# Performance work log

Hardware: AMD Instinct MI355X
Metric: run time of the kernel (lower is better)

The kernel has to match this reference:

```python
import jax, jax.numpy as jnp
import numpy as np

D_MODEL = 1024
N_HEADS = 1  # original code's final .view only works for n_heads == 1 (unprojected V has dim d_model per head)
HEAD_DIM = D_MODEL // N_HEADS
N, LEN_Q, LEN_IN = 8, 1024, 4096


def setup_inputs() -> dict:
    key = jax.random.key(0)
    ks = jax.random.split(key, 7)
    s = 1.0 / np.sqrt(D_MODEL)  # linear-layer style init scale
    return {
        "query": jax.random.normal(ks[0], (N, LEN_Q, D_MODEL), dtype=jnp.float32),
        "input_flatten": jax.random.normal(ks[1], (N, LEN_IN, D_MODEL), dtype=jnp.float32),
        "input_padding_mask": jax.random.randint(ks[2], (N, LEN_IN), 0, 2).astype(bool),
        "Wq": jax.random.normal(ks[3], (D_MODEL, D_MODEL), dtype=jnp.float32) * s,
        "bq": jnp.zeros((D_MODEL,), dtype=jnp.float32),
        "Wk": jax.random.normal(ks[4], (D_MODEL, D_MODEL), dtype=jnp.float32) * s,
        "bk": jnp.zeros((D_MODEL,), dtype=jnp.float32),
        "Wo": jax.random.normal(ks[5], (D_MODEL, D_MODEL), dtype=jnp.float32) * s,
        "bo": jnp.zeros((D_MODEL,), dtype=jnp.float32),
    }


def reference(query, input_flatten, input_padding_mask, Wq, bq, Wk, bk, Wo, bo):
    n, len_q, _ = query.shape
    len_in = input_flatten.shape[1]
    # projections (torch Linear: x @ W^T + b)
    Q = (query @ Wq.T + bq).reshape(n, len_q, N_HEADS, HEAD_DIM).transpose(0, 2, 1, 3)
    K = (input_flatten @ Wk.T + bk).reshape(n, len_in, N_HEADS, HEAD_DIM).transpose(0, 2, 1, 3)
    # unscaled attention scores (original applies no 1/sqrt(d))
    scores = jnp.einsum("nhqd,nhkd->nhqk", Q, K)  # (N, H, Lq, Lk)
    scores = jnp.where(input_padding_mask[:, None, None, :], -jnp.inf, scores)
    attn = jax.nn.softmax(scores, axis=-1)
    # V is the UNPROJECTED input, replicated per head (dim = d_model)
    V = jnp.broadcast_to(input_flatten[:, None], (n, N_HEADS, len_in, D_MODEL))
    out = jnp.einsum("nhql,nhld->nhqd", attn, V)  # (N, H, Lq, d_model)
    out = out.transpose(0, 2, 1, 3).reshape(n, len_q, D_MODEL)  # valid since N_HEADS == 1
    return out @ Wo.T + bo
```

## Files before the change

### kernel.cpp

```cpp
#include <hip/hip_runtime.h>
#include <math.h>


using short8 = __attribute__((ext_vector_type(8))) short;
using f32x4  = __attribute__((ext_vector_type(4))) float;

__device__ inline ushort f2h_u(float f) {
    _Float16 h = (_Float16)f;
    return __builtin_bit_cast(ushort, h);
}
__device__ inline float h2f(ushort u) {
    return (float)__builtin_bit_cast(_Float16, u);
}
__device__ inline void split2h(float x, ushort& h, ushort& l) {
    const ushort hu = f2h_u(x);
    h = hu;
    l = f2h_u(x - h2f(hu));
}

__global__ __launch_bounds__(256)
void bias_proj_k(const float* __restrict__ bq, const float* __restrict__ Wk,
                 float* __restrict__ bp)
{
    const int j = blockIdx.x * 256 + threadIdx.x;
    float s = 0.f;
    for (int d = 0; d < 1024; ++d) s = fmaf(bq[d], Wk[d * 1024 + j], s);
    bp[j] = s;
}

__global__ __launch_bounds__(256)
void split_k(const float* __restrict__ x, ushort* __restrict__ hi,
             ushort* __restrict__ lo, int n4)
{
    for (int i = blockIdx.x * 256 + threadIdx.x; i < n4; i += gridDim.x * 256) {
        const float4 v = reinterpret_cast<const float4*>(x)[i];
        ushort4 h, l;
        split2h(v.x, h.x, l.x); split2h(v.y, h.y, l.y);
        split2h(v.z, h.z, l.z); split2h(v.w, h.w, l.w);
        reinterpret_cast<ushort4*>(hi)[i] = h;
        if (lo) reinterpret_cast<ushort4*>(lo)[i] = l;
    }
}

__global__ __launch_bounds__(256)
void trans_split_k(const float* __restrict__ in, ushort* __restrict__ oh,
                   ushort* __restrict__ ol, int R, int C)
{
    __shared__ float ts[32][33];
    const int t = threadIdx.x, tx = t & 31, tg = t >> 5;
    const int r0 = blockIdx.y * 32, c0 = blockIdx.x * 32;
    #pragma unroll
    for (int i = 0; i < 4; ++i) {
        const int r = tg * 4 + i;
        ts[r][tx] = in[(size_t)(r0 + r) * C + c0 + tx];
    }
    __syncthreads();
    #pragma unroll
    for (int i = 0; i < 4; ++i) {
        const int c = tg * 4 + i;
        ushort h, l; split2h(ts[tx][c], h, l);
        const size_t o = (size_t)(c0 + c) * R + r0 + tx;
        oh[o] = h;
        if (ol) ol[o] = l;
    }
}

__global__ __launch_bounds__(256)
void prep_input_k(const float* __restrict__ in, ushort* __restrict__ i2,
                  ushort* __restrict__ vt, int LI, int D, long long bs)
{
    __shared__ float ts[32][33];
    const int t = threadIdx.x;
    const int tx8 = t & 7, ty = t >> 3;
    const int r0 = blockIdx.y * 32, c0 = blockIdx.x * 32;
    const long long z = blockIdx.z;
    in += z * bs; i2 += z * bs * 2; vt += z * bs;

    const float4 v = *reinterpret_cast<const float4*>(
        &in[(size_t)(r0 + ty) * D + c0 + tx8 * 4]);
    ushort4 h, l;
    split2h(v.x, h.x, l.x); split2h(v.y, h.y, l.y);
    split2h(v.z, h.z, l.z); split2h(v.w, h.w, l.w);
    const size_t rbase = (size_t)(r0 + ty) * 2048 + c0 + tx8 * 4;
    *reinterpret_cast<ushort4*>(&i2[rbase]) = h;
    *reinterpret_cast<ushort4*>(&i2[rbase + 1024]) = l;
    ts[ty][tx8 * 4 + 0] = v.x; ts[ty][tx8 * 4 + 1] = v.y;
    ts[ty][tx8 * 4 + 2] = v.z; ts[ty][tx8 * 4 + 3] = v.w;
    __syncthreads();
    const int tx = t & 31, tg = t >> 5;
    #pragma unroll
    for (int i = 0; i < 4; ++i) {
        const int c = tg * 4 + i;
        vt[(size_t)(c0 + c) * LI + r0 + tx] = f2h_u(ts[tx][c]);
    }
}

__global__ __launch_bounds__(256)
void softmax_f16_k(const float* __restrict__ S, const int* __restrict__ mask,
                   ushort* __restrict__ P)
{
    const int t = threadIdx.x;
    const size_t row = (size_t)blockIdx.y * gridDim.x + blockIdx.x;
    const float* srow = S + row * 4096;
    ushort* prow = P + row * 4096;
    mask += (size_t)blockIdx.y * 4096;
    float4 v[4];
    float lmax = -INFINITY;
    #pragma unroll
    for (int c = 0; c < 4; ++c) {
        const int idx = c * 1024 + t * 4;
        v[c] = *reinterpret_cast<const float4*>(&srow[idx]);
        const int4 m4 = *reinterpret_cast<const int4*>(&mask[idx]);
        if (m4.x) v[c].x = -INFINITY;
        if (m4.y) v[c].y = -INFINITY;
        if (m4.z) v[c].z = -INFINITY;
        if (m4.w) v[c].w = -INFINITY;
        lmax = fmaxf(lmax, fmaxf(fmaxf(v[c].x, v[c].y), fmaxf(v[c].z, v[c].w)));
    }
    #pragma unroll
    for (int off = 32; off > 0; off >>= 1)
        lmax = fmaxf(lmax, __shfl_xor(lmax, off));
    __shared__ float redm[4], reds[4];
    if ((t & 63) == 0) redm[t >> 6] = lmax;
    __syncthreads();
    const float bmax = fmaxf(fmaxf(redm[0], redm[1]), fmaxf(redm[2], redm[3]));
    float lsum = 0.f;
    #pragma unroll
    for (int c = 0; c < 4; ++c) {
        v[c].x = __expf(v[c].x - bmax);
        v[c].y = __expf(v[c].y - bmax);
        v[c].z = __expf(v[c].z - bmax);
        v[c].w = __expf(v[c].w - bmax);
        lsum += (v[c].x + v[c].y) + (v[c].z + v[c].w);
    }
    #pragma unroll
    for (int off = 32; off > 0; off >>= 1)
        lsum += __shfl_xor(lsum, off);
    if ((t & 63) == 0) reds[t >> 6] = lsum;
    __syncthreads();
    const float Z = (reds[0] + reds[1]) + (reds[2] + reds[3]);
    const float inv = 1.0f / Z;
    #pragma unroll
    for (int c = 0; c < 4; ++c) {
        const int idx = c * 1024 + t * 4;
        ushort4 o;
        o.x = f2h_u(v[c].x * inv); o.y = f2h_u(v[c].y * inv);
        o.z = f2h_u(v[c].z * inv); o.w = f2h_u(v[c].w * inv);
        *reinterpret_cast<ushort4*>(&prow[idx]) = o;
    }
}

template<int TR>
__device__ inline void stage_one(const ushort* __restrict__ g, int ld, int r0,
                                 int k0, ushort* ldsbase, int w, int l)
{
    constexpr int ISS = TR / 64;
    #pragma unroll
    for (int q = 0; q < ISS; ++q) {
        const int idx = (w * ISS + q) * 64 + l;
        const int row = idx >> 2;
        const int gslot = (idx & 3) ^ ((idx >> 3) & 3);
        const ushort* src = g + (size_t)(r0 + row) * ld + k0 + gslot * 8;
        ushort* dst = ldsbase + (size_t)(w * ISS + q) * 512;
        __builtin_amdgcn_global_load_lds(
            (const __attribute__((address_space(1))) void*)src,
            (__attribute__((address_space(3))) void*)dst, 16, 0, 0);
    }
}

template<int BM, int BN, int AS, int BS, int OUTMODE>
__global__ __launch_bounds__(256, 2)
void mfma_gemm_k(const ushort* __restrict__ Ah, const ushort* __restrict__ Al,
                 const ushort* __restrict__ Bh, const ushort* __restrict__ Bl,
                 const float* __restrict__ bias,
                 float* __restrict__ Cf, ushort* __restrict__ Ch,
                 ushort* __restrict__ Cl,
                 int K, int lda, int ldb, int ldc,
                 long long bsA, long long bsB, long long bsC)
{
    constexpr int FM = BM / 32, FN = BN / 32;
    constexpr int AU = AS * BM * 32;
    constexpr int TILE_U = AU + BS * BN * 32;
    __shared__ __align__(16) ushort lds[2][TILE_U];

    const long long zb = blockIdx.z;
    Ah += zb * bsA; Bh += zb * bsB;
    if constexpr (AS == 2) Al += zb * bsA;
    if constexpr (BS == 2) Bl += zb * bsB;

    const int t = threadIdx.x;
    const int l = t & 63, w = t >> 6;
    const int lr = l & 15, ls = l >> 4;
    const int i0 = blockIdx.y * BM, j0 = blockIdx.x * BN;
    const int wr = (w >> 1) * (BM / 2), wc = (w & 1) * (BN / 2);
    const int swu = (ls ^ ((lr >> 1) & 3)) * 8;

    f32x4 acc[FM][FN] = {};
    const int nk = K >> 5;

    auto stage = [&](int buf, int kt) {
        const int k0 = kt << 5;
        ushort* base = &lds[buf][0];
        stage_one<BM>(Ah, lda, i0, k0, base, w, l);
        if constexpr (AS == 2) stage_one<BM>(Al, lda, i0, k0, base + BM * 32, w, l);
        stage_one<BN>(Bh, ldb, j0, k0, base + AU, w, l);
        if constexpr (BS == 2) stage_one<BN>(Bl, ldb, j0, k0, base + AU + BN * 32, w, l);
    };

    stage(0, 0);
    for (int kt = 0; kt < nk; ++kt) {
        __syncthreads();
        const int buf = kt & 1;
        if (kt + 1 < nk) stage(buf ^ 1, kt + 1);
        const ushort* base = &lds[buf][0];

        short8 ah[FM], bh[FN];
        #pragma unroll
        for (int fi = 0; fi < FM; ++fi)
            ah[fi] = *reinterpret_cast<const short8*>(
                base + (wr + fi * 16 + lr) * 32 + swu);
        #pragma unroll
        for (int fj = 0; fj < FN; ++fj)
            bh[fj] = *reinterpret_cast<const short8*>(
                base + AU + (wc + fj * 16 + lr) * 32 + swu);

        #pragma unroll
        for (int fi = 0; fi < FM; ++fi)
            #pragma unroll
            for (int fj = 0; fj < FN; ++fj)
                acc[fi][fj] = __builtin_amdgcn_mfma_f32_16x16x32_f16(
                    ah[fi], bh[fj], acc[fi][fj], 0, 0, 0);

        if constexpr (BS == 2) {
            short8 bl[FN];
            #pragma unroll
            for (int fj = 0; fj < FN; ++fj)
                bl[fj] = *reinterpret_cast<const short8*>(
                    base + AU + BN * 32 + (wc + fj * 16 + lr) * 32 + swu);
            #pragma unroll
            for (int fi = 0; fi < FM; ++fi)
                #pragma unroll
                for (int fj = 0; fj < FN; ++fj)
                    acc[fi][fj] = __builtin_amdgcn_mfma_f32_16x16x32_f16(
                        ah[fi], bl[fj], acc[fi][fj], 0, 0, 0);
        }
        if constexpr (AS == 2) {
            short8 al[FM];
            #pragma unroll
            for (int fi = 0; fi < FM; ++fi)
                al[fi] = *reinterpret_cast<const short8*>(
                    base + BM * 32 + (wr + fi * 16 + lr) * 32 + swu);
            #pragma unroll
            for (int fi = 0; fi < FM; ++fi)
                #pragma unroll
                for (int fj = 0; fj < FN; ++fj)
                    acc[fi][fj] = __builtin_amdgcn_mfma_f32_16x16x32_f16(
                        al[fi], bh[fj], acc[fi][fj], 0, 0, 0);
        }
    }

    #pragma unroll
    for (int fj = 0; fj < FN; ++fj) {
        const int gc = j0 + wc + fj * 16 + lr;
        const float bv = bias ? bias[gc] : 0.0f;
        #pragma unroll
        for (int fi = 0; fi < FM; ++fi) {
            const int gr = i0 + wr + fi * 16 + ls * 4;
            #pragma unroll
            for (int r = 0; r < 4; ++r) {
                const float v = acc[fi][fj][r] + bv;
                const size_t o = zb * bsC + (size_t)(gr + r) * ldc + gc;
                if constexpr (OUTMODE == 0) {
                    Cf[o] = v;
                } else if constexpr (OUTMODE == 1) {
                    Ch[o] = f2h_u(v);
                } else {
                    ushort h, lo2; split2h(v, h, lo2);
                    Ch[o] = h;
                    Cl[o] = lo2;
                }
            }
        }
    }
}

__global__ __launch_bounds__(512, 2)
void gemm256_k(const ushort* __restrict__ A, const ushort* __restrict__ B,
               float* __restrict__ Cf,
               int K, int lda, int ldb, int ldc, int kmaskA,
               long long bsA, long long bsB, long long bsC,
               int gx, int gy)
{
    extern __shared__ ushort lds[];
    const int tid = threadIdx.x;
    const int w = tid >> 6, l = tid & 63;
    const int lr = l & 15, ls = l >> 4;
    const int wr = (w >> 2) * 128, wc = (w & 3) * 64;

    const int nwg = gridDim.x;
    const int q8 = nwg >> 3;
    const int swz = (blockIdx.x & 7) * q8 + (blockIdx.x >> 3);
    const int pt = gx * gy;
    const int z = swz / pt;
    const int r2 = swz - z * pt;
    const int by = r2 / gx, bx = r2 - by * gx;
    const int i0 = by * 256, j0 = bx * 256;

    A += (long long)z * bsA;
    B += (long long)z * bsB;

    const int swu = (ls ^ ((lr >> 1) & 3)) * 8;
    const int kmaskB = K - 1;

    f32x4 acc[8][4] = {};
    const int nk = K >> 6;

    auto stage = [&](const ushort* g, int ld, int row0, int kbase, int kmask, int reg) {
        ushort* base = lds + reg * 8192;
        #pragma unroll
        for (int q2 = 0; q2 < 2; ++q2) {
            const int s = (w * 2 + q2) * 64 + l;
            const int row = s >> 2;
            const int gslot = (s & 3) ^ ((row >> 1) & 3);
            const ushort* src = g + (size_t)(row0 + row) * ld + ((kbase + gslot * 8) & kmask);
            __builtin_amdgcn_global_load_lds(
                (const __attribute__((address_space(1))) void*)src,
                (__attribute__((address_space(3))) void*)(base + s * 8), 16, 0, 0);
        }
    };

    stage(A, lda, i0, 0,  kmaskA, 0);
    stage(B, ldb, j0, 0,  kmaskB, 1);
    stage(A, lda, i0, 32, kmaskA, 2);
    stage(B, ldb, j0, 32, kmaskB, 3);
    stage(A, lda, i0, 64, kmaskA, 4);
    stage(B, ldb, j0, 64, kmaskB, 5);
    asm volatile("s_waitcnt vmcnt(8)" ::: "memory");
    __builtin_amdgcn_s_barrier();

#define MFMA16(MH)                                                          \
    __builtin_amdgcn_s_setprio(1);                                          \
    _Pragma("unroll")                                                       \
    for (int i = 0; i < 4; ++i)                                             \
        _Pragma("unroll")                                                   \
        for (int j = 0; j < 4; ++j)                                         \
            acc[(MH)*4 + i][j] = __builtin_amdgcn_mfma_f32_16x16x32_f16(    \
                af[i], bf[j], acc[(MH)*4 + i][j], 0, 0, 0);                 \
    __builtin_amdgcn_s_setprio(0);

    for (int t = 0; t < nk; ++t) {
        const int b = t & 1;
        const int t1 = (t + 1 < nk) ? t + 1 : 0;
        const int t2 = (t + 2 < nk) ? t + 2 : t + 2 - nk;
        const int cb = b * 4, rb = (b ^ 1) * 4;
        const ushort* RA0 = lds + (cb + 0) * 8192;
        const ushort* RB0 = lds + (cb + 1) * 8192;
        const ushort* RA1 = lds + (cb + 2) * 8192;
        const ushort* RB1 = lds + (cb + 3) * 8192;

        short8 af[4], bf[4];

        #pragma unroll
        for (int i = 0; i < 4; ++i)
            af[i] = *reinterpret_cast<const short8*>(RA0 + (wr + i * 16 + lr) * 32 + swu);
        #pragma unroll
        for (int j = 0; j < 4; ++j)
            bf[j] = *reinterpret_cast<const short8*>(RB0 + (wc + j * 16 + lr) * 32 + swu);
        stage(A, lda, i0, t1 * 64 + 32, kmaskA, rb + 2);
        __builtin_amdgcn_s_barrier();
        asm volatile("s_waitcnt lgkmcnt(0)" ::: "memory");
        __builtin_amdgcn_sched_barrier(0);
        MFMA16(0)
        __builtin_amdgcn_s_barrier();

        #pragma unroll
        for (int i = 0; i < 4; ++i)
            af[i] = *reinterpret_cast<const short8*>(RA0 + (wr + 64 + i * 16 + lr) * 32 + swu);
        stage(B, ldb, j0, t1 * 64 + 32, kmaskB, rb + 3);
        asm volatile("s_waitcnt vmcnt(8)" ::: "memory");
        __builtin_amdgcn_s_barrier();
        asm volatile("s_waitcnt lgkmcnt(0)" ::: "memory");
        __builtin_amdgcn_sched_barrier(0);
        MFMA16(1)
        __builtin_amdgcn_s_barrier();

        #pragma unroll
        for (int i = 0; i < 4; ++i)
            af[i] = *reinterpret_cast<const short8*>(RA1 + (wr + i * 16 + lr) * 32 + swu);
        #pragma unroll
        for (int j = 0; j < 4; ++j)
            bf[j] = *reinterpret_cast<const short8*>(RB1 + (wc + j * 16 + lr) * 32 + swu);
        stage(A, lda, i0, t2 * 64, kmaskA, cb + 0);
        __builtin_amdgcn_s_barrier();
        asm volatile("s_waitcnt lgkmcnt(0)" ::: "memory");
        __builtin_amdgcn_sched_barrier(0);
        MFMA16(0)
        __builtin_amdgcn_s_barrier();

        #pragma unroll
        for (int i = 0; i < 4; ++i)
            af[i] = *reinterpret_cast<const short8*>(RA1 + (wr + 64 + i * 16 + lr) * 32 + swu);
        stage(B, ldb, j0, t2 * 64, kmaskB, cb + 1);
        asm volatile("s_waitcnt vmcnt(8)" ::: "memory");
        __builtin_amdgcn_s_barrier();
        asm volatile("s_waitcnt lgkmcnt(0)" ::: "memory");
        __builtin_amdgcn_sched_barrier(0);
        MFMA16(1)
        __builtin_amdgcn_s_barrier();
    }
#undef MFMA16

    asm volatile("s_waitcnt vmcnt(0)" ::: "memory");

    #pragma unroll
    for (int a = 0; a < 8; ++a) {
        const int gr0 = i0 + wr + (a >> 2) * 64 + (a & 3) * 16 + ls * 4;
        #pragma unroll
        for (int j = 0; j < 4; ++j) {
            const int gc = j0 + wc + j * 16 + lr;
            #pragma unroll
            for (int r = 0; r < 4; ++r)
                Cf[(long long)z * bsC + (size_t)(gr0 + r) * ldc + gc] = acc[a][j][r];
        }
    }
}

extern "C" void kernel_launch(void* const* d_in, const int* in_sizes, int n_in,
                              void* d_out, int out_size, void* d_ws, size_t ws_size,
                              hipStream_t stream)
{
    (void)in_sizes; (void)n_in; (void)out_size;
    const int NB = 8, LQ = 1024, LI = 4096, D = 1024;
    const long long sQD = (long long)LQ * D;
    const long long sID = (long long)LI * D;
    const long long sQI = (long long)LQ * LI;

    const float* query = (const float*)d_in[0];
    const float* input = (const float*)d_in[1];
    const int* mask = (const int*)d_in[2];
    const float* Wq = (const float*)d_in[3];
    const float* bq = (const float*)d_in[4];
    const float* Wk = (const float*)d_in[5];
    const float* Wo = (const float*)d_in[7];
    const float* bo = (const float*)d_in[8];
    float* out = (float*)d_out;

    dim3 blk(256);

    (void)hipFuncSetAttribute(reinterpret_cast<const void*>(gemm256_k),
                              hipFuncAttributeMaxDynamicSharedMemorySize, 131072);

    char* p = (char*)d_ws;
    auto alloc = [&](size_t bytes) {
        char* r = p; p += (bytes + 255) & ~(size_t)255; return r;
    };
    ushort* qh   = (ushort*)alloc((size_t)NB * sQD * 2);
    ushort* WqTh = (ushort*)alloc((size_t)D * D * 2);
    ushort* WqTl = (ushort*)alloc((size_t)D * D * 2);
    ushort* WkTh = (ushort*)alloc((size_t)D * D * 2);
    ushort* WkTl = (ushort*)alloc((size_t)D * D * 2);
    ushort* WTh  = (ushort*)alloc((size_t)D * D * 2);
    ushort* WTl  = (ushort*)alloc((size_t)D * D * 2);
    float*  bp   = (float*) alloc((size_t)D * 4);
    ushort* Qh   = (ushort*)alloc((size_t)NB * sQD * 2);
    ushort* Ob   = (ushort*)alloc((size_t)NB * sQD * 2);
    ushort* Wob  = (ushort*)alloc((size_t)D * D * 2);
    char* tail = p;

    ushort* in2 = (ushort*)alloc((size_t)NB * sID * 2 * 2);
    ushort* VT  = (ushort*)alloc((size_t)NB * sID * 2);
    float*  S   = (float*) alloc((size_t)NB * sQI * 4);
    ushort* Pb  = (ushort*)alloc((size_t)NB * sQI * 2);
    const bool full = (size_t)(p - (char*)d_ws) <= ws_size;
    if (!full) {
        p = tail;
        in2 = (ushort*)alloc((size_t)sID * 2 * 2);
        VT  = (ushort*)alloc((size_t)sID * 2);
        S   = (float*) alloc((size_t)sQI * 4);
        Pb  = (ushort*)alloc((size_t)sQI * 2);
    }

    trans_split_k<<<dim3(32, 32), blk, 0, stream>>>(Wq, WqTh, WqTl, D, D);
    trans_split_k<<<dim3(32, 32), blk, 0, stream>>>(Wk, WkTh, WkTl, D, D);
    bias_proj_k<<<dim3(4), blk, 0, stream>>>(bq, Wk, bp);
    mfma_gemm_k<64, 64, 2, 2, 2><<<dim3(16, 16, 1), blk, 0, stream>>>(
        WkTh, WkTl, WqTh, WqTl, nullptr, nullptr, WTh, WTl, D, D, D, D, 0, 0, 0);
    split_k<<<dim3(2048), blk, 0, stream>>>(query, qh, nullptr, NB * (int)sQD / 4);
    split_k<<<dim3(1024), blk, 0, stream>>>(Wo, Wob, nullptr, D * D / 4);
    mfma_gemm_k<128, 128, 1, 2, 1><<<dim3(D / 128, NB * LQ / 128, 1), blk, 0, stream>>>(
        qh, nullptr, WTh, WTl, bp, nullptr, Qh, nullptr, D, D, D, D, 0, 0, 0);

    if (full) {
        prep_input_k<<<dim3(D / 32, LI / 32, NB), blk, 0, stream>>>(
            input, in2, VT, LI, D, sID);
        gemm256_k<<<dim3(16 * 4 * NB), dim3(512), 131072, stream>>>(
            Qh, in2, S, 2048, D, 2048, LI, 1023, sQD, sID * 2, sQI, 16, 4);
        softmax_f16_k<<<dim3(LQ, NB), blk, 0, stream>>>(S, mask, Pb);
        mfma_gemm_k<128, 128, 1, 1, 1><<<dim3(D / 128, LQ / 128, NB), blk, 0, stream>>>(
            Pb, nullptr, VT, nullptr, nullptr, nullptr, Ob, nullptr,
            LI, LI, LI, D, sQI, sID, sQD);
    } else {
        for (int b = 0; b < NB; ++b) {
            const float* in_b = input + (size_t)b * sID;
            prep_input_k<<<dim3(D / 32, LI / 32, 1), blk, 0, stream>>>(
                in_b, in2, VT, LI, D, 0);
            gemm256_k<<<dim3(16 * 4), dim3(512), 131072, stream>>>(
                Qh + (size_t)b * sQD, in2, S, 2048, D, 2048, LI, 1023,
                0, 0, 0, 16, 4);
            softmax_f16_k<<<dim3(LQ, 1), blk, 0, stream>>>(S, mask + (size_t)b * LI, Pb);
            mfma_gemm_k<128, 128, 1, 1, 1><<<dim3(D / 128, LQ / 128, 1), blk, 0, stream>>>(
                Pb, nullptr, VT, nullptr, nullptr, nullptr,
                Ob + (size_t)b * sQD, nullptr, LI, LI, LI, D, 0, 0, 0);
        }
    }
    mfma_gemm_k<128, 128, 1, 1, 0><<<dim3(D / 128, NB * LQ / 128, 1), blk, 0, stream>>>(
        Ob, nullptr, Wob, nullptr, bo, out, nullptr, nullptr, D, D, D, D, 0, 0, 0);
}
```

Before: 541.2 us.

## Double-buffer MFMA register fragments to overlap LDS reads with matrix ops

Restructures the 256x256 GEMM main loop so the A/B fragments for the next MFMA group are read from LDS into a second register set while the current group runs. Full lgkmcnt(0) waits become partial waits, and the vmcnt waits move so global-to-LDS staging still completes before reuse. Launch bounds drop from 2 to 1 workgroup per CU so the extra fragment registers fit. The cost is lower occupancy and more fragile waitcnt accounting, which could give stale reads if the counts are wrong.

```diff
diff --git a/kernel.cpp b/kernel.cpp
--- a/kernel.cpp
+++ b/kernel.cpp
@@ -284,7 +284,7 @@
     }
 }
 
-__global__ __launch_bounds__(512, 2)
+__global__ __launch_bounds__(512, 1)
 void gemm256_k(const ushort* __restrict__ A, const ushort* __restrict__ B,
                float* __restrict__ Cf,
                int K, int lda, int ldb, int ldc, int kmaskA,
@@ -313,6 +313,7 @@
     const int kmaskB = K - 1;
 
     f32x4 acc[8][4] = {};
+    short8 afC[4], afN[4], bfC[4], bfN[4];
     const int nk = K >> 6;
 
     auto stage = [&](const ushort* g, int ld, int row0, int kbase, int kmask, int reg) {
@@ -328,6 +329,18 @@
                 (__attribute__((address_space(3))) void*)(base + s * 8), 16, 0, 0);
         }
     };
+    auto rdA = [&](short8* dst, const ushort* R, int mh) {
+        #pragma unroll
+        for (int i = 0; i < 4; ++i)
+            dst[i] = *reinterpret_cast<const short8*>(
+                R + (wr + mh * 64 + i * 16 + lr) * 32 + swu);
+    };
+    auto rdB = [&](short8* dst, const ushort* R) {
+        #pragma unroll
+        for (int j = 0; j < 4; ++j)
+            dst[j] = *reinterpret_cast<const short8*>(
+                R + (wc + j * 16 + lr) * 32 + swu);
+    };
 
     stage(A, lda, i0, 0,  kmaskA, 0);
     stage(B, ldb, j0, 0,  kmaskB, 1);
@@ -337,15 +350,17 @@
     stage(B, ldb, j0, 64, kmaskB, 5);
     asm volatile("s_waitcnt vmcnt(8)" ::: "memory");
     __builtin_amdgcn_s_barrier();
-
-#define MFMA16(MH)                                                          \
+    rdA(afC, lds + 0 * 8192, 0);
+    rdB(bfC, lds + 1 * 8192);
+
+#define MFMA16(MH, AF, BF)                                                  \
     __builtin_amdgcn_s_setprio(1);                                          \
     _Pragma("unroll")                                                       \
     for (int i = 0; i < 4; ++i)                                             \
         _Pragma("unroll")                                                   \
         for (int j = 0; j < 4; ++j)                                         \
             acc[(MH)*4 + i][j] = __builtin_amdgcn_mfma_f32_16x16x32_f16(    \
-                af[i], bf[j], acc[(MH)*4 + i][j], 0, 0, 0);                 \
+                AF[i], BF[j], acc[(MH)*4 + i][j], 0, 0, 0);                 \
     __builtin_amdgcn_s_setprio(0);
 
     for (int t = 0; t < nk; ++t) {
@@ -354,63 +369,50 @@
         const int t2 = (t + 2 < nk) ? t + 2 : t + 2 - nk;
         const int cb = b * 4, rb = (b ^ 1) * 4;
         const ushort* RA0 = lds + (cb + 0) * 8192;
-        const ushort* RB0 = lds + (cb + 1) * 8192;
         const ushort* RA1 = lds + (cb + 2) * 8192;
         const ushort* RB1 = lds + (cb + 3) * 8192;
-
-        short8 af[4], bf[4];
-
-        #pragma unroll
-        for (int i = 0; i < 4; ++i)
-            af[i] = *reinterpret_cast<const short8*>(RA0 + (wr + i * 16 + lr) * 32 + swu);
-        #pragma unroll
-        for (int j = 0; j < 4; ++j)
-            bf[j] = *reinterpret_cast<const short8*>(RB0 + (wc + j * 16 + lr) * 32 + swu);
+        const ushort* NA0 = lds + (rb + 0) * 8192;
+        const ushort* NB0 = lds + (rb + 1) * 8192;
+
+        rdA(afN, RA0, 1);
         stage(A, lda, i0, t1 * 64 + 32, kmaskA, rb + 2);
         __builtin_amdgcn_s_barrier();
-        asm volatile("s_waitcnt lgkmcnt(0)" ::: "memory");
+        asm volatile("s_waitcnt lgkmcnt(4)" ::: "memory");
         __builtin_amdgcn_sched_barrier(0);
-        MFMA16(0)
-        __builtin_amdgcn_s_barrier();
-
-        #pragma unroll
-        for (int i = 0; i < 4; ++i)
-            af[i] = *reinterpret_cast<const short8*>(RA0 + (wr + 64 + i * 16 + lr) * 32 + swu);
+        MFMA16(0, afC, bfC)
+        asm volatile("s_waitcnt vmcnt(6)" ::: "memory");
+        __builtin_amdgcn_s_barrier();
+
+        rdA(afC, RA1, 0);
+        rdB(bfN, RB1);
         stage(B, ldb, j0, t1 * 64 + 32, kmaskB, rb + 3);
-        asm volatile("s_waitcnt vmcnt(8)" ::: "memory");
-        __builtin_amdgcn_s_barrier();
-        asm volatile("s_waitcnt lgkmcnt(0)" ::: "memory");
+        __builtin_amdgcn_s_barrier();
+        asm volatile("s_waitcnt lgkmcnt(8)" ::: "memory");
         __builtin_amdgcn_sched_barrier(0);
-        MFMA16(1)
-        __builtin_amdgcn_s_barrier();
-
-        #pragma unroll
-        for (int i = 0; i < 4; ++i)
-            af[i] = *reinterpret_cast<const short8*>(RA1 + (wr + i * 16 + lr) * 32 + swu);
-        #pragma unroll
-        for (int j = 0; j < 4; ++j)
-            bf[j] = *reinterpret_cast<const short8*>(RB1 + (wc + j * 16 + lr) * 32 + swu);
+        MFMA16(1, afN, bfC)
+        __builtin_amdgcn_s_barrier();
+
+        rdA(afN, RA1, 1);
         stage(A, lda, i0, t2 * 64, kmaskA, cb + 0);
         __builtin_amdgcn_s_barrier();
-        asm volatile("s_waitcnt lgkmcnt(0)" ::: "memory");
+        asm volatile("s_waitcnt lgkmcnt(4)" ::: "memory");
         __builtin_amdgcn_sched_barrier(0);
-        MFMA16(0)
-        __builtin_amdgcn_s_barrier();
-
-        #pragma unroll
-        for (int i = 0; i < 4; ++i)
-            af[i] = *reinterpret_cast<const short8*>(RA1 + (wr + 64 + i * 16 + lr) * 32 + swu);
+        MFMA16(0, afC, bfN)
+        asm volatile("s_waitcnt vmcnt(6)" ::: "memory");
+        __builtin_amdgcn_s_barrier();
+
+        rdA(afC, NA0, 0);
+        rdB(bfC, NB0);
         stage(B, ldb, j0, t2 * 64, kmaskB, cb + 1);
-        asm volatile("s_waitcnt vmcnt(8)" ::: "memory");
-        __builtin_amdgcn_s_barrier();
-        asm volatile("s_waitcnt lgkmcnt(0)" ::: "memory");
+        __builtin_amdgcn_s_barrier();
+        asm volatile("s_waitcnt lgkmcnt(8)" ::: "memory");
         __builtin_amdgcn_sched_barrier(0);
-        MFMA16(1)
+        MFMA16(1, afN, bfN)
         __builtin_amdgcn_s_barrier();
     }
 #undef MFMA16
 
-    asm volatile("s_waitcnt vmcnt(0)" ::: "memory");
+    asm volatile("s_waitcnt vmcnt(0) lgkmcnt(0)" ::: "memory");
 
     #pragma unroll
     for (int a = 0; a < 8; ++a) {
```

After: 544.3 us. Within noise of the previous version (+0.6%).
